# Optimization experiments

Measured on AMD Instinct MI355X. Metric: run time of the kernel, lower is better.

## Reference

```python
import jax, jax.numpy as jnp
import numpy as np

M_ROWS, K, N = 4096, 4096, 4096
DIVFACTOR = 1.0 / (127.0 * 127.0)


def setup_inputs() -> dict:
    key = jax.random.key(0)
    k1, k2, k3, k4, k5 = jax.random.split(key, 5)
    # quantized activations and weights, int8 range
    x = jax.random.randint(k1, (M_ROWS, K), -128, 128, dtype=jnp.int32).astype(jnp.int8)
    scale_x = jnp.abs(jax.random.normal(k2, (M_ROWS,), dtype=jnp.float32)) * 0.01
    weight_int8 = jax.random.randint(k3, (N, K), -128, 128, dtype=jnp.int32).astype(jnp.int8)
    scale_w = jnp.abs(jax.random.normal(k4, (N,), dtype=jnp.float32)) * 0.01
    bias = (jax.random.normal(k5, (N,), dtype=jnp.float32) * 0.01).astype(jnp.float16)
    return {"x": x, "scale_x": scale_x, "weight_int8": weight_int8, "scale_w": scale_w, "bias": bias}


def reference(x, scale_x, weight_int8, scale_w, bias):
    # int8 @ int8^T accumulated (reference path computes in fp32, like torch .float())
    acc = jnp.matmul(x.astype(jnp.float32), weight_int8.T.astype(jnp.float32))  # [M, N]
    out = scale_w[None, :] * (scale_x[:, None] * (acc * DIVFACTOR))
    out = out + bias[None, :].astype(jnp.float32)  # bias promoted fp16->fp32, as in torch
    return out.astype(jnp.float16)
```

## Files before the change

### kernel.cpp

```cpp
#include <hip/hip_runtime.h>
#include <hip/hip_fp16.h>

typedef int v4i  __attribute__((ext_vector_type(4)));
typedef const unsigned __attribute__((address_space(1)))* gas_t;
typedef unsigned __attribute__((address_space(3)))* las_t;

#define DIVFACTOR (1.0f / 16129.0f)

__device__ __forceinline__ unsigned pack4(int4 v) {
    return (unsigned)(v.x & 0xFF) | ((unsigned)(v.y & 0xFF) << 8) |
           ((unsigned)(v.z & 0xFF) << 16) | ((unsigned)v.w << 24);
}

__device__ __forceinline__ void gload16(const void* g, void* l) {
    __builtin_amdgcn_global_load_lds((gas_t)g, (las_t)l, 16, 0, 0);
}

__global__ __launch_bounds__(256) void pack_kernel(
    const int* __restrict__ x, const int* __restrict__ w, uint4* __restrict__ ws)
{
    const int u   = blockIdx.x * 256 + threadIdx.x;
    const int s   = u & 7;
    const int row = (u >> 3) & 127;
    const int h   = (u >> 10) & 1;
    const int kt  = (u >> 11) & 31;
    const int p   = u >> 16;
    const int* src = (blockIdx.y == 0) ? x : w;
    uint4* dst = ws + (size_t)blockIdx.y * 1048576;

    const int grow = p * 256 + h * 128 + row;
    const int4* sp = (const int4*)(src + (size_t)grow * 4096 + kt * 128 + s * 16);
    int4 s0 = sp[0], s1 = sp[1], s2 = sp[2], s3 = sp[3];
    uint4 d = make_uint4(pack4(s0), pack4(s1), pack4(s2), pack4(s3));
    dst[(((size_t)((p * 32 + kt) * 2 + h)) << 10) + row * 8 + (s ^ (row & 7))] = d;
}

__global__ __launch_bounds__(512, 1) void i8gemm_8ph(
    const uint4* __restrict__ Ap, const uint4* __restrict__ Bp,
    const float* __restrict__ scale_x, const float* __restrict__ scale_w,
    const void* __restrict__ bias, float* __restrict__ out)
{
    __shared__ uint4 ldsq[8192];
    char* ldsb = (char*)ldsq;

    const int bid = blockIdx.x;
    const int swb = ((bid & 7) << 5) | (bid >> 3);
    const int bx  = swb & 15;
    const int by  = swb >> 4;

    const int t    = threadIdx.x;
    const int lane = t & 63;
    const int wid  = t >> 6;
    const int wr   = wid >> 2;
    const int wc   = wid & 3;
    const int r    = lane & 15;
    const int g    = lane >> 4;

    const uint4* aBase = Ap + (size_t)by * 65536 + t;
    const uint4* bBase = Bp + (size_t)bx * 65536 + t;

    const int sl0 = ((g ^ (r & 7)) << 4);
    const int sl1 = (((4 + g) ^ (r & 7)) << 4);
    const int aoff0 = wr * 16384 + r * 128 + sl0;
    const int aoff1 = wr * 16384 + r * 128 + sl1;
    const int boff0 = 32768 + (wc >> 1) * 16384 + ((wc & 1) * 64 + r) * 128 + sl0;
    const int boff1 = 32768 + (wc >> 1) * 16384 + ((wc & 1) * 64 + r) * 128 + sl1;

#define ARD(BUF,M,KS) (*(const v4i*)(ldsb + (BUF)*65536 + aoff##KS + (M)*2048))
#define BRD(BUF,N,KS) (*(const v4i*)(ldsb + (BUF)*65536 + boff##KS + (N)*2048))

#define STAGE(KT, MAT, HALF, BUF) do{ \
    const uint4* s_ = ((MAT) ? bBase : aBase) + (KT)*2048 + (HALF)*1024; \
    char* d_ = ldsb + (BUF)*65536 + (MAT)*32768 + (HALF)*16384 + t*16; \
    gload16((const void*)s_, (void*)d_); \
    gload16((const void*)(s_ + 512), (void*)(d_ + 8192)); \
}while(0)

#define BAR asm volatile("s_barrier" ::: "memory")
#define VM4 asm volatile("s_waitcnt vmcnt(4)" ::: "memory")
#define VM0 asm volatile("s_waitcnt vmcnt(0)" ::: "memory")
#define VM8 asm volatile("s_waitcnt vmcnt(8)" ::: "memory")

#define RD_A2(BUF,M0) do{ \
    afr[M0][0]   = ARD(BUF,M0,0);   afr[M0][1]   = ARD(BUF,M0,1); \
    afr[(M0)+1][0] = ARD(BUF,(M0)+1,0); afr[(M0)+1][1] = ARD(BUF,(M0)+1,1); \
}while(0)

#define RD_B8(BUF,ARR) do{ \
    _Pragma("unroll") for (int n_ = 0; n_ < 4; ++n_) { \
        ARR[n_][0] = BRD(BUF,n_,0); ARR[n_][1] = BRD(BUF,n_,1); } \
}while(0)

#define CLUSTER(ARR,MA,MB) do{ \
    __builtin_amdgcn_s_setprio(1); \
    _Pragma("unroll") for (int n_ = 0; n_ < 4; ++n_) { \
        acc[MA][n_] = __builtin_amdgcn_mfma_i32_16x16x64_i8(afr[MA][0], ARR[n_][0], acc[MA][n_], 0,0,0); \
        acc[MA][n_] = __builtin_amdgcn_mfma_i32_16x16x64_i8(afr[MA][1], ARR[n_][1], acc[MA][n_], 0,0,0); \
        acc[MB][n_] = __builtin_amdgcn_mfma_i32_16x16x64_i8(afr[MB][0], ARR[n_][0], acc[MB][n_], 0,0,0); \
        acc[MB][n_] = __builtin_amdgcn_mfma_i32_16x16x64_i8(afr[MB][1], ARR[n_][1], acc[MB][n_], 0,0,0); } \
    __builtin_amdgcn_s_setprio(0); \
}while(0)

#define ITER(KB, STEADY) do{ \
    RD_A2(0,0); STAGE((KB)+1,1,0,1); BAR; CLUSTER(bfrA,0,1); BAR;              \
    RD_A2(0,2); STAGE((KB)+1,1,1,1); BAR; CLUSTER(bfrA,2,3); BAR;              \
    RD_A2(0,4); if (STEADY) STAGE((KB)+2,1,0,0); BAR; CLUSTER(bfrA,4,5); BAR;  \
    RD_A2(0,6); if (STEADY) { STAGE((KB)+2,1,1,0); VM4; } else { VM0; } \
    BAR; RD_B8(1,bfrB); CLUSTER(bfrA,6,7); BAR;                                \
    RD_A2(1,0); RD_A2(1,2); if (STEADY) STAGE((KB)+2,0,0,0); BAR; CLUSTER(bfrB,0,1); BAR;  \
    RD_A2(1,4); RD_A2(1,6); if (STEADY) { STAGE((KB)+2,0,1,0); VM4; } \
    BAR; if (STEADY) RD_B8(0,bfrA); CLUSTER(bfrB,2,3); BAR;                    \
    if (STEADY) STAGE((KB)+3,0,0,1); BAR; CLUSTER(bfrB,4,5); BAR;              \
    if (STEADY) { STAGE((KB)+3,0,1,1); VM4; } BAR; CLUSTER(bfrB,6,7); BAR;     \
}while(0)

    v4i acc[8][4];
    #pragma unroll
    for (int m = 0; m < 8; ++m)
        #pragma unroll
        for (int n = 0; n < 4; ++n) acc[m][n] = (v4i){0, 0, 0, 0};
    v4i afr[8][2], bfrA[4][2], bfrB[4][2];

    STAGE(0,1,0,0); STAGE(0,1,1,0);
    STAGE(0,0,0,0); STAGE(0,0,1,0);
    STAGE(1,0,0,1); STAGE(1,0,1,1);
    VM8; BAR;
    RD_B8(0,bfrA);
    VM4; BAR;

    for (int i = 0; i < 15; ++i) { ITER(2 * i, 1); }
    ITER(30, 0);

#undef ITER
#undef CLUSTER
#undef RD_B8
#undef RD_A2
#undef VM8
#undef VM0
#undef VM4
#undef BAR
#undef STAGE
#undef BRD
#undef ARD

    const float p0  = ((const float*)bias)[0];
    const float ap0 = fabsf(p0);
    const bool bias_is_f32 = (ap0 >= 1e-6f && ap0 <= 1.0f);

    float swv[4], bvv[4];
    #pragma unroll
    for (int n = 0; n < 4; ++n) {
        int col = bx * 256 + wc * 64 + n * 16 + r;
        swv[n] = scale_w[col];
        bvv[n] = bias_is_f32 ? ((const float*)bias)[col]
                             : __half2float(((const __half*)bias)[col]);
    }

    #pragma unroll
    for (int m = 0; m < 8; ++m) {
        float sxr[4];
        #pragma unroll
        for (int q = 0; q < 4; ++q)
            sxr[q] = scale_x[by * 256 + wr * 128 + m * 16 + g * 4 + q] * DIVFACTOR;
        #pragma unroll
        for (int q = 0; q < 4; ++q) {
            int row = by * 256 + wr * 128 + m * 16 + g * 4 + q;
            #pragma unroll
            for (int n = 0; n < 4; ++n) {
                int col = bx * 256 + wc * 64 + n * 16 + r;
                float v = (float)acc[m][n][q] * sxr[q] * swv[n] + bvv[n];
                out[(size_t)row * 4096 + col] = __half2float(__float2half(v));
            }
        }
    }
}

__global__ __launch_bounds__(256) void i8gemm_kernel(
    const int* __restrict__ x, const int* __restrict__ w,
    const float* __restrict__ scale_x, const float* __restrict__ scale_w,
    const void* __restrict__ bias, float* __restrict__ out)
{
    __shared__ int lds[4096];
    const int t = threadIdx.x, bx = blockIdx.x, by = blockIdx.y;
    const int lane = t & 63, wid = t >> 6, wr = wid >> 1, wc = wid & 1;
    const int th = t >> 4, tl = t & 15;
    const int* aptr = x + (size_t)(by * 128 + th) * 4096 + tl * 4;
    const int* bptr = w + (size_t)(bx * 128 + th) * 4096 + tl * 4;
    const int wbase = th * 16 + (tl ^ (((th >> 1) & 3) << 2));
    const int r = lane & 15, g = lane >> 4;
    const int sw4 = (r >> 1) & 3;
    const int a_rd = (wr * 64 + r) * 16 + ((g ^ sw4) << 2);
    const int b_rd = 2048 + (wc * 64 + r) * 16 + ((g ^ sw4) << 2);

    v4i acc[4][4];
    #pragma unroll
    for (int m = 0; m < 4; ++m)
        #pragma unroll
        for (int n = 0; n < 4; ++n) acc[m][n] = (v4i){0, 0, 0, 0};

    int4 va[8], vb[8];
    #pragma unroll
    for (int j = 0; j < 8; ++j) { va[j] = *(const int4*)(aptr + j * 65536); vb[j] = *(const int4*)(bptr + j * 65536); }

    for (int kt = 0; kt < 64; ++kt) {
        __syncthreads();
        #pragma unroll
        for (int j = 0; j < 8; ++j) {
            lds[wbase + j * 256]        = (int)pack4(va[j]);
            lds[2048 + wbase + j * 256] = (int)pack4(vb[j]);
        }
        __syncthreads();
        if (kt < 63) {
            const int* ap = aptr + (kt + 1) * 64;
            const int* bp = bptr + (kt + 1) * 64;
            #pragma unroll
            for (int j = 0; j < 8; ++j) { va[j] = *(const int4*)(ap + j * 65536); vb[j] = *(const int4*)(bp + j * 65536); }
        }
        v4i af[4], bf[4];
        #pragma unroll
        for (int m = 0; m < 4; ++m) af[m] = *(const v4i*)&lds[a_rd + m * 256];
        #pragma unroll
        for (int n = 0; n < 4; ++n) bf[n] = *(const v4i*)&lds[b_rd + n * 256];
        #pragma unroll
        for (int m = 0; m < 4; ++m)
            #pragma unroll
            for (int n = 0; n < 4; ++n)
                acc[m][n] = __builtin_amdgcn_mfma_i32_16x16x64_i8(af[m], bf[n], acc[m][n], 0, 0, 0);
    }

    const float p0 = ((const float*)bias)[0];
    const float ap0 = fabsf(p0);
    const bool bias_is_f32 = (ap0 >= 1e-6f && ap0 <= 1.0f);
    float sxv[4][4];
    #pragma unroll
    for (int m = 0; m < 4; ++m)
        #pragma unroll
        for (int q = 0; q < 4; ++q)
            sxv[m][q] = scale_x[by * 128 + wr * 64 + m * 16 + g * 4 + q] * DIVFACTOR;
    float swv[4], bvv[4];
    #pragma unroll
    for (int n = 0; n < 4; ++n) {
        int col = bx * 128 + wc * 64 + n * 16 + r;
        swv[n] = scale_w[col];
        bvv[n] = bias_is_f32 ? ((const float*)bias)[col] : __half2float(((const __half*)bias)[col]);
    }
    #pragma unroll
    for (int m = 0; m < 4; ++m)
        #pragma unroll
        for (int q = 0; q < 4; ++q) {
            int row = by * 128 + wr * 64 + m * 16 + g * 4 + q;
            float s = sxv[m][q];
            #pragma unroll
            for (int n = 0; n < 4; ++n) {
                int col = bx * 128 + wc * 64 + n * 16 + r;
                float v = (float)acc[m][n][q] * s * swv[n] + bvv[n];
                out[(size_t)row * 4096 + col] = __half2float(__float2half(v));
            }
        }
}

extern "C" void kernel_launch(void* const* d_in, const int* in_sizes, int n_in,
                              void* d_out, int out_size, void* d_ws, size_t ws_size,
                              hipStream_t stream) {
    const int*   x   = (const int*)d_in[0];
    const float* sx  = (const float*)d_in[1];
    const int*   w   = (const int*)d_in[2];
    const float* sw  = (const float*)d_in[3];
    const void*  bi  = d_in[4];
    float*       out = (float*)d_out;
    (void)in_sizes; (void)n_in; (void)out_size;

    if (ws_size >= (size_t)33554432) {
        uint4* ws = (uint4*)d_ws;
        hipLaunchKernelGGL(pack_kernel, dim3(4096, 2, 1), dim3(256, 1, 1), 0, stream, x, w, ws);
        hipLaunchKernelGGL(i8gemm_8ph, dim3(256, 1, 1), dim3(512, 1, 1), 0, stream,
                           ws, ws + 1048576, sx, sw, bi, out);
    } else {
        hipLaunchKernelGGL(i8gemm_kernel, dim3(32, 32, 1), dim3(256, 1, 1), 0, stream,
                           x, w, sx, sw, bi, out);
    }
}
```

Before: 231.4 us.

## Double-buffer A fragments in registers and reschedule LDS staging in GEMM loop

The main loop now keeps A fragments in two ping-pong register sets. Each cluster's MFMAs consume fragments that were read from LDS during the previous phase, so LDS reads no longer sit directly ahead of their consumers. The global-to-LDS staging order and the vmcnt waits are reshuffled, including a new vmcnt(2) point and a smaller prologue. The pack kernel switches to nontemporal loads. The restaged A half may race with reads of the same buffer if the barrier and wait placement is wrong, and the lower register footprint of the A fragments could shift the allocation.

```diff
diff --git a/kernel.cpp b/kernel.cpp
--- a/kernel.cpp
+++ b/kernel.cpp
@@ -7,6 +7,10 @@
 
 #define DIVFACTOR (1.0f / 16129.0f)
 
+__device__ __forceinline__ unsigned pack4v(v4i v) {
+    return (unsigned)(v[0] & 0xFF) | ((unsigned)(v[1] & 0xFF) << 8) |
+           ((unsigned)(v[2] & 0xFF) << 16) | ((unsigned)v[3] << 24);
+}
 __device__ __forceinline__ unsigned pack4(int4 v) {
     return (unsigned)(v.x & 0xFF) | ((unsigned)(v.y & 0xFF) << 8) |
            ((unsigned)(v.z & 0xFF) << 16) | ((unsigned)v.w << 24);
@@ -29,9 +33,12 @@
     uint4* dst = ws + (size_t)blockIdx.y * 1048576;
 
     const int grow = p * 256 + h * 128 + row;
-    const int4* sp = (const int4*)(src + (size_t)grow * 4096 + kt * 128 + s * 16);
-    int4 s0 = sp[0], s1 = sp[1], s2 = sp[2], s3 = sp[3];
-    uint4 d = make_uint4(pack4(s0), pack4(s1), pack4(s2), pack4(s3));
+    const v4i* sp = (const v4i*)(src + (size_t)grow * 4096 + kt * 128 + s * 16);
+    v4i s0 = __builtin_nontemporal_load(sp + 0);
+    v4i s1 = __builtin_nontemporal_load(sp + 1);
+    v4i s2 = __builtin_nontemporal_load(sp + 2);
+    v4i s3 = __builtin_nontemporal_load(sp + 3);
+    uint4 d = make_uint4(pack4v(s0), pack4v(s1), pack4v(s2), pack4v(s3));
     dst[(((size_t)((p * 32 + kt) * 2 + h)) << 10) + row * 8 + (s ^ (row & 7))] = d;
 }
 
@@ -78,12 +85,12 @@
 
 #define BAR asm volatile("s_barrier" ::: "memory")
 #define VM4 asm volatile("s_waitcnt vmcnt(4)" ::: "memory")
+#define VM2 asm volatile("s_waitcnt vmcnt(2)" ::: "memory")
 #define VM0 asm volatile("s_waitcnt vmcnt(0)" ::: "memory")
-#define VM8 asm volatile("s_waitcnt vmcnt(8)" ::: "memory")
-
-#define RD_A2(BUF,M0) do{ \
-    afr[M0][0]   = ARD(BUF,M0,0);   afr[M0][1]   = ARD(BUF,M0,1); \
-    afr[(M0)+1][0] = ARD(BUF,(M0)+1,0); afr[(M0)+1][1] = ARD(BUF,(M0)+1,1); \
+
+#define RD_A2TO(BUF,M0,DST) do{ \
+    DST[0][0] = ARD(BUF,M0,0);     DST[0][1] = ARD(BUF,M0,1); \
+    DST[1][0] = ARD(BUF,(M0)+1,0); DST[1][1] = ARD(BUF,(M0)+1,1); \
 }while(0)
 
 #define RD_B8(BUF,ARR) do{ \
@@ -91,27 +98,28 @@
         ARR[n_][0] = BRD(BUF,n_,0); ARR[n_][1] = BRD(BUF,n_,1); } \
 }while(0)
 
-#define CLUSTER(ARR,MA,MB) do{ \
+#define CLUSTER(BARR,AFR,M0) do{ \
     __builtin_amdgcn_s_setprio(1); \
     _Pragma("unroll") for (int n_ = 0; n_ < 4; ++n_) { \
-        acc[MA][n_] = __builtin_amdgcn_mfma_i32_16x16x64_i8(afr[MA][0], ARR[n_][0], acc[MA][n_], 0,0,0); \
-        acc[MA][n_] = __builtin_amdgcn_mfma_i32_16x16x64_i8(afr[MA][1], ARR[n_][1], acc[MA][n_], 0,0,0); \
-        acc[MB][n_] = __builtin_amdgcn_mfma_i32_16x16x64_i8(afr[MB][0], ARR[n_][0], acc[MB][n_], 0,0,0); \
-        acc[MB][n_] = __builtin_amdgcn_mfma_i32_16x16x64_i8(afr[MB][1], ARR[n_][1], acc[MB][n_], 0,0,0); } \
+        acc[M0][n_]     = __builtin_amdgcn_mfma_i32_16x16x64_i8(AFR[0][0], BARR[n_][0], acc[M0][n_], 0,0,0); \
+        acc[M0][n_]     = __builtin_amdgcn_mfma_i32_16x16x64_i8(AFR[0][1], BARR[n_][1], acc[M0][n_], 0,0,0); \
+        acc[(M0)+1][n_] = __builtin_amdgcn_mfma_i32_16x16x64_i8(AFR[1][0], BARR[n_][0], acc[(M0)+1][n_], 0,0,0); \
+        acc[(M0)+1][n_] = __builtin_amdgcn_mfma_i32_16x16x64_i8(AFR[1][1], BARR[n_][1], acc[(M0)+1][n_], 0,0,0); } \
     __builtin_amdgcn_s_setprio(0); \
 }while(0)
 
 #define ITER(KB, STEADY) do{ \
-    RD_A2(0,0); STAGE((KB)+1,1,0,1); BAR; CLUSTER(bfrA,0,1); BAR;              \
-    RD_A2(0,2); STAGE((KB)+1,1,1,1); BAR; CLUSTER(bfrA,2,3); BAR;              \
-    RD_A2(0,4); if (STEADY) STAGE((KB)+2,1,0,0); BAR; CLUSTER(bfrA,4,5); BAR;  \
-    RD_A2(0,6); if (STEADY) { STAGE((KB)+2,1,1,0); VM4; } else { VM0; } \
-    BAR; RD_B8(1,bfrB); CLUSTER(bfrA,6,7); BAR;                                \
-    RD_A2(1,0); RD_A2(1,2); if (STEADY) STAGE((KB)+2,0,0,0); BAR; CLUSTER(bfrB,0,1); BAR;  \
-    RD_A2(1,4); RD_A2(1,6); if (STEADY) { STAGE((KB)+2,0,1,0); VM4; } \
-    BAR; if (STEADY) RD_B8(0,bfrA); CLUSTER(bfrB,2,3); BAR;                    \
-    if (STEADY) STAGE((KB)+3,0,0,1); BAR; CLUSTER(bfrB,4,5); BAR;              \
-    if (STEADY) { STAGE((KB)+3,0,1,1); VM4; } BAR; CLUSTER(bfrB,6,7); BAR;     \
+    RD_A2TO(0,2,afrN); STAGE((KB)+1,1,0,1); STAGE((KB)+1,0,1,1); BAR; CLUSTER(bR0,afrP,0); BAR;   \
+    RD_A2TO(0,4,afrP); STAGE((KB)+1,1,1,1); BAR; CLUSTER(bR0,afrN,2); BAR;                         \
+    RD_A2TO(0,6,afrN); if (STEADY) STAGE((KB)+2,1,0,0); BAR; CLUSTER(bR0,afrP,4); BAR;             \
+    if (STEADY) { STAGE((KB)+2,1,1,0); VM4; } else { VM0; } \
+    BAR; RD_B8(1,bR1); RD_A2TO(1,0,afrP); CLUSTER(bR0,afrN,6); BAR;                                \
+    RD_A2TO(1,2,afrN); if (STEADY) STAGE((KB)+2,0,0,0); BAR; CLUSTER(bR1,afrP,0); BAR;             \
+    RD_A2TO(1,4,afrP); if (STEADY) { STAGE((KB)+2,0,1,0); VM4; } \
+    BAR; if (STEADY) RD_B8(0,bR0); CLUSTER(bR1,afrN,2); BAR;                                       \
+    RD_A2TO(1,6,afrN); BAR; CLUSTER(bR1,afrP,4); BAR;                                              \
+    if (STEADY) { STAGE((KB)+3,0,0,1); VM2; } \
+    BAR; if (STEADY) RD_A2TO(0,0,afrP); CLUSTER(bR1,afrN,6); BAR;                                  \
 }while(0)
 
     v4i acc[8][4];
@@ -119,14 +127,12 @@
     for (int m = 0; m < 8; ++m)
         #pragma unroll
         for (int n = 0; n < 4; ++n) acc[m][n] = (v4i){0, 0, 0, 0};
-    v4i afr[8][2], bfrA[4][2], bfrB[4][2];
-
-    STAGE(0,1,0,0); STAGE(0,1,1,0);
-    STAGE(0,0,0,0); STAGE(0,0,1,0);
-    STAGE(1,0,0,1); STAGE(1,0,1,1);
-    VM8; BAR;
-    RD_B8(0,bfrA);
-    VM4; BAR;
+    v4i afrP[2][2], afrN[2][2], bR0[4][2], bR1[4][2];
+
+    STAGE(0,1,0,0); STAGE(0,1,1,0); STAGE(0,0,0,0); STAGE(0,0,1,0);
+    STAGE(1,0,0,1);
+    VM2; BAR;
+    RD_B8(0,bR0); RD_A2TO(0,0,afrP);
 
     for (int i = 0; i < 15; ++i) { ITER(2 * i, 1); }
     ITER(30, 0);
@@ -134,9 +140,9 @@
 #undef ITER
 #undef CLUSTER
 #undef RD_B8
-#undef RD_A2
-#undef VM8
+#undef RD_A2TO
 #undef VM0
+#undef VM2
 #undef VM4
 #undef BAR
 #undef STAGE
```

Result: no change. 233.7 us (+1.0%).
